# Performance work log

Hardware: AMD Instinct MI355X
Metric: run time of the kernel (lower is better)

## Reference

```python
import jax, jax.numpy as jnp
import numpy as np
from jax import lax

# hyperparams (match init_kwargs)
DIM = 192      # dim
QK = 192       # qk_dim
HEADS = 8
GS = 128       # group_size
MLP = 384      # mlp_dim
M = 64         # num_tokens
B, H, W = 4, 128, 128


def setup_inputs() -> dict:
    key = jax.random.key(0)
    ks = jax.random.split(key, 12)
    def n(k, sh, sc=0.02):
        return jax.random.normal(k, sh, dtype=jnp.float32) * sc
    return {
        "x": n(ks[0], (B, DIM, H, W), 1.0),
        "ln_g": jnp.ones((DIM,), jnp.float32),
        "ln_b": jnp.zeros((DIM,), jnp.float32),
        "Wq": n(ks[1], (DIM, QK)),
        "Wk": n(ks[2], (DIM, QK)),
        "Wv": n(ks[3], (DIM, DIM)),
        "Wproj": n(ks[4], (DIM, DIM)),
        "Wkg": n(ks[5], (DIM, QK)),      # IRCA global-key projection of means
        "Wvg": n(ks[6], (DIM, DIM)),     # IRCA global-value projection of means
        "means": n(ks[7], (M, DIM), 1.0),  # token dictionary buffer
        "Wconv": n(ks[8], (DIM, DIM)),   # 1x1 conv (no bias) as matrix
        "mlp_ln_g": jnp.ones((DIM,), jnp.float32),
        "mlp_ln_b": jnp.zeros((DIM,), jnp.float32),
        "W_fc1": n(ks[9], (DIM, MLP)),
        "dw": n(ks[10], (MLP, 1, 3, 3)),  # depthwise 3x3 in ConvFFN
        "W_fc2": n(ks[11], (MLP, DIM)),
    }


def _ln(x, g, b, eps=1e-5):
    mu = x.mean(-1, keepdims=True)
    var = ((x - mu) ** 2).mean(-1, keepdims=True)
    return (x - mu) * lax.rsqrt(var + eps) * g + b


def _attn(q, k, v):
    scale = q.shape[-1] ** -0.5
    s = jnp.einsum('...qd,...kd->...qk', q, k) * scale
    p = jax.nn.softmax(s, axis=-1)
    return jnp.einsum('...qk,...kd->...qd', p, v)


def reference(x, ln_g, ln_b, Wq, Wk, Wv, Wproj, Wkg, Wvg, means,
              Wconv, mlp_ln_g, mlp_ln_b, W_fc1, dw, W_fc2):
    b, C, h, w = x.shape
    N = h * w
    xt = x.reshape(b, C, N).transpose(0, 2, 1)          # b n c
    residual = xt
    xn = _ln(xt, ln_g, ln_b)

    # IRCA: per-head global K/V from the token dictionary (means)
    kg = (means @ Wkg).reshape(M, HEADS, QK // HEADS).transpose(1, 0, 2)   # h m dq
    vg = (means @ Wvg).reshape(M, HEADS, C // HEADS).transpose(1, 0, 2)    # h m dv

    # cluster assignment (no-grad): cosine sim to means, argsort by cluster id
    xs = lax.stop_gradient(xn)
    ms = lax.stop_gradient(means)
    xs_n = xs / (jnp.linalg.norm(xs, axis=-1, keepdims=True) + 1e-12)
    ms_n = ms / (jnp.linalg.norm(ms, axis=-1, keepdims=True) + 1e-12)
    belong = jnp.argmax(xs_n @ ms_n.T, axis=-1)          # b n
    idx = jnp.argsort(belong, axis=-1)                   # b n, cluster-sorted order

    # IASA: project, gather into cluster-sorted order
    q = jnp.take_along_axis(xn @ Wq, idx[:, :, None], axis=1)
    k = jnp.take_along_axis(xn @ Wk, idx[:, :, None], axis=1)
    v = jnp.take_along_axis(xn @ Wv, idx[:, :, None], axis=1)

    gs = min(N, GS)
    ng = (N + gs - 1) // gs
    pad_n = ng * gs - N
    pq = jnp.concatenate([q, q[:, N - pad_n:N][:, ::-1]], axis=1)
    pq = pq.reshape(b, ng, gs, HEADS, -1).transpose(0, 1, 3, 2, 4)  # b ng h gs dq

    def windows(t):
        tr = jnp.concatenate([t, t[:, N - pad_n - gs:N][:, ::-1]], axis=1)  # len ng*gs+gs
        t1 = tr[:, :ng * gs].reshape(b, ng, gs, -1)
        t2 = tr[:, gs:].reshape(b, ng, gs, -1)
        tw = jnp.concatenate([t1, t2], axis=2)           # b ng 2gs c
        return tw.reshape(b, ng, 2 * gs, HEADS, -1).transpose(0, 1, 3, 2, 4)

    kw, vw = windows(k), windows(v)
    out1 = _attn(pq, kw, vw)                             # local overlapping windows
    out2 = _attn(pq, kg[None, None], vg[None, None])     # global dictionary attention
    out = (out1 + out2).transpose(0, 1, 3, 2, 4).reshape(b, ng * gs, C)[:, :N]

    # scatter back to original token order (idx is a permutation)
    inv = jnp.argsort(idx, axis=-1)
    out = jnp.take_along_axis(out, inv[:, :, None], axis=1)
    out = (out @ Wproj) @ Wconv                           # proj + 1x1 conv (no bias)
    xt = residual + out

    # PreNorm ConvFFN: LN -> fc1 -> depthwise 3x3 -> GELU -> fc2, residual
    h1 = _ln(xt, mlp_ln_g, mlp_ln_b) @ W_fc1              # b n mlp
    himg = h1.transpose(0, 2, 1).reshape(b, MLP, h, w)
    dwc = lax.conv_general_dilated(himg, dw, (1, 1), 'SAME',
                                   feature_group_count=MLP,
                                   dimension_numbers=('NCHW', 'OIHW', 'NCHW'))
    h2 = jax.nn.gelu(dwc.reshape(b, MLP, N).transpose(0, 2, 1))
    xt = xt + h2 @ W_fc2
    return xt.transpose(0, 2, 1).reshape(b, C, h, w)
```

## Files before the change

### kernel.cpp

```cpp
#include <hip/hip_runtime.h>

using u16 = unsigned short;
using u32 = unsigned int;
typedef __attribute__((ext_vector_type(8))) short short8;
typedef __attribute__((ext_vector_type(4))) short s16x4;
typedef __attribute__((ext_vector_type(4))) float f32x4;
typedef __attribute__((ext_vector_type(2))) float f32x2;
typedef __attribute__((ext_vector_type(4))) u16 u16x4;
typedef __attribute__((ext_vector_type(4))) u32 u32x4;

constexpr int CB   = 4;
constexpr int CC   = 192;
constexpr int CN   = 16384;
constexpr int BN   = CB * CN;
constexpr int CMLP = 384;

__device__ __forceinline__ float b2f(u16 u){ return __uint_as_float(((u32)u) << 16); }
__device__ __forceinline__ u16 f2b(float f){
  u32 u = __float_as_uint(f);
  u32 r = (u + 0x7FFFu + ((u >> 16) & 1u)) >> 16;
  return (u16)r;
}
__device__ __forceinline__ short8 ld8(const u16* p) {
  s16x4 a = *(const s16x4*)p;
  s16x4 b = *(const s16x4*)(p + 4);
  short8 r;
  r[0]=a[0]; r[1]=a[1]; r[2]=a[2]; r[3]=a[3];
  r[4]=b[0]; r[5]=b[1]; r[6]=b[2]; r[7]=b[3];
  return r;
}
__device__ __forceinline__ u32 pk_bf16(float lo, float hi) {
  u32 r;
  asm("v_cvt_pk_bf16_f32 %0, %1, %2" : "=v"(r) : "v"(lo), "v"(hi));
  return r;
}
__device__ __forceinline__ float exp2_fast(float x) {
  float r;
  asm("v_exp_f32 %0, %1" : "=v"(r) : "v"(x));
  return r;
}
__device__ __forceinline__ void gl_lds16(const u16* g, u16* l) {
  __builtin_amdgcn_global_load_lds(
      (const __attribute__((address_space(1))) void*)(const void*)g,
      (__attribute__((address_space(3))) void*)(void*)l, 16, 0, 0);
}

__global__ __launch_bounds__(256) void ln_k(const float* __restrict__ src,
    const float* __restrict__ gg, const float* __restrict__ bb, u16* __restrict__ out,
    const u16* __restrict__ msnT, int* __restrict__ belong)
{
  __shared__ float t[64 * 193];
  __shared__ float sg[192], sb[192];
  __shared__ float smu[64], srs[64];
  const int tid = threadIdx.x;
  const int blk = blockIdx.x;
  const int b = blk >> 8;
  const int n0 = (blk & 255) * 64;
  if (tid < 192) { sg[tid] = gg[tid]; sb[tid] = bb[tid]; }
  const size_t sbase = ((size_t)b * CC) * CN + n0;
  #pragma unroll
  for (int it = 0; it < 48; ++it) {
    int c = it * 4 + (tid >> 6);
    int tok = tid & 63;
    t[tok * 193 + c] = src[sbase + (size_t)c * CN + tok];
  }
  __syncthreads();
  {
    int tok = tid >> 2, sub = tid & 3;
    float s = 0.f, sq = 0.f;
    #pragma unroll
    for (int i = 0; i < 48; ++i) {
      float v = t[tok * 193 + sub * 48 + i];
      s += v; sq += v * v;
    }
    s  += __shfl_xor(s, 1);  s  += __shfl_xor(s, 2);
    sq += __shfl_xor(sq, 1); sq += __shfl_xor(sq, 2);
    float mu = s * (1.f / 192.f);
    float var = fmaxf(sq * (1.f / 192.f) - mu * mu, 0.f);
    float rs = rsqrtf(var + 1e-5f);
    if (sub == 0) { smu[tok] = mu; srs[tok] = rs; }
  }
  __syncthreads();
  const size_t obase = ((size_t)(b * CN + n0)) * CC;
  #pragma unroll
  for (int it = 0; it < 48; ++it) {
    int e = it * 256 + tid;
    int tk = e / 192, c = e % 192;
    float v = (t[tk * 193 + c] - smu[tk]) * srs[tk] * sg[c] + sb[c];
    out[obase + (size_t)tk * CC + c] = f2b(v);
  }

  {
    const int wv = tid >> 6, lane = tid & 63;
    const int l15 = lane & 15, g4 = lane >> 4, q8 = g4 * 8;
    const int tok = wv * 16 + l15;
    const float mu = smu[tok], rs = srs[tok];
    short8 afm[6];
    #pragma unroll
    for (int ks = 0; ks < 6; ++ks) {
      u32x4 qq;
      #pragma unroll
      for (int j = 0; j < 4; ++j) {
        int c = ks * 32 + q8 + 2 * j;
        float v0 = (t[tok * 193 + c]     - mu) * rs * sg[c]     + sb[c];
        float v1 = (t[tok * 193 + c + 1] - mu) * rs * sg[c + 1] + sb[c + 1];
        qq[j] = pk_bf16(v0, v1);
      }
      afm[ks] = __builtin_bit_cast(short8, qq);
    }
    f32x4 sacc[4];
    #pragma unroll
    for (int ct = 0; ct < 4; ++ct) {
      sacc[ct] = 0.f;
      const u16* pM = msnT + (ct * 16 + l15) * 192 + q8;
      short8 mf[6];
      #pragma unroll
      for (int ks = 0; ks < 6; ++ks) mf[ks] = *(const short8*)(pM + ks * 32);
      #pragma unroll
      for (int ks = 0; ks < 6; ++ks)
        sacc[ct] = __builtin_amdgcn_mfma_f32_16x16x32_bf16(afm[ks], mf[ks], sacc[ct], 0, 0, 0);
    }
    #pragma unroll
    for (int r = 0; r < 4; ++r) {
      float bv = -3e38f; int bi = 1 << 30;
      #pragma unroll
      for (int ct = 0; ct < 4; ++ct) {
        float v = sacc[ct][r];
        int ci = ct * 16 + l15;
        if (v > bv || (v == bv && ci < bi)) { bv = v; bi = ci; }
      }
      #pragma unroll
      for (int d = 1; d < 16; d <<= 1) {
        float ov = __shfl_xor(bv, d);
        int   oi = __shfl_xor(bi, d);
        if (ov > bv || (ov == bv && oi < bi)) { bv = ov; bi = oi; }
      }
      if (l15 == 0) belong[b * CN + n0 + wv * 16 + g4 * 4 + r] = bi;
    }
  }
}

__global__ __launch_bounds__(256) void gemmQ_k(const u16* __restrict__ A,
    const u16* __restrict__ Wt, u16* __restrict__ qkv)
{
  __shared__ __attribute__((aligned(16))) u16 lA[64 * 192];
  const float QSC = 0.20412414523193154f * 1.4426950408889634f;
  const int tid = threadIdx.x;
  const int row0 = blockIdx.x * 64;
  const int wv = tid >> 6, lane = tid & 63;
  const int l15 = lane & 15, g4 = lane >> 4, q8 = g4 * 8;
  const int colw = wv * 144;

  #pragma unroll
  for (int j = 0; j < 6; ++j) {
    int C = (wv * 6 + j) * 64 + lane;
    int r = C / 24;
    int c = C - r * 24;
    gl_lds16(A + (size_t)(row0 + r) * 192 + c * 8, lA + (wv * 6 + j) * 512);
  }
  __syncthreads();
  short8 af[4][6];
  #pragma unroll
  for (int rt = 0; rt < 4; ++rt)
    #pragma unroll
    for (int ks = 0; ks < 6; ++ks)
      af[rt][ks] = *(const short8*)(lA + (rt * 16 + l15) * 192 + ks * 32 + q8);

  #pragma unroll
  for (int jc = 0; jc < 9; ++jc) {
    const u16* pW = Wt + (size_t)(colw + jc * 16 + l15) * 192 + q8;
    short8 wf[6];
    #pragma unroll
    for (int ks = 0; ks < 6; ++ks) wf[ks] = *(const short8*)(pW + ks * 32);
    f32x4 acc[4];
    #pragma unroll
    for (int rt = 0; rt < 4; ++rt) acc[rt] = 0.f;
    #pragma unroll
    for (int ks = 0; ks < 6; ++ks)
      #pragma unroll
      for (int rt = 0; rt < 4; ++rt)
        acc[rt] = __builtin_amdgcn_mfma_f32_16x16x32_bf16(af[rt][ks], wf[ks], acc[rt], 0, 0, 0);
    int col = colw + jc * 16 + l15;
    const float sc = (colw + jc * 16 < 192) ? QSC : 1.f;
    #pragma unroll
    for (int rt = 0; rt < 4; ++rt) {
      int row = row0 + rt * 16 + g4 * 4;
      #pragma unroll
      for (int r = 0; r < 4; ++r)
        qkv[(size_t)(row + r) * 576 + col] = f2b(acc[rt][r] * sc);
    }
  }
}

__global__ __launch_bounds__(192) void prep_means_k(const float* __restrict__ means,
    const float* __restrict__ Wkg, const float* __restrict__ Wvg,
    u16* __restrict__ msnT, float* __restrict__ kg, float* __restrict__ vg)
{
  __shared__ float sv[192];
  __shared__ float red[192];
  const int m = blockIdx.x, c = threadIdx.x;
  float v = means[m * 192 + c];
  sv[c] = v; red[c] = v * v;
  __syncthreads();
  for (int s = 96; s >= 3; s >>= 1) {
    if (c < s) red[c] += red[c + s];
    __syncthreads();
  }
  if (c == 0) red[0] = 1.f / (sqrtf(red[0] + red[1] + red[2]) + 1e-12f);
  __syncthreads();
  float scale = red[0];
  msnT[m * 192 + c] = f2b(v * scale);
  float a1 = 0.f, a2 = 0.f;
  for (int cc = 0; cc < 192; ++cc) {
    float mv = sv[cc];
    a1 += mv * Wkg[cc * 192 + c];
    a2 += mv * Wvg[cc * 192 + c];
  }
  int h = c / 24, d = c % 24;
  kg[h * (64 * 24) + m * 24 + d] = a1;
  vg[h * (64 * 24) + m * 24 + d] = a2;
}

__global__ __launch_bounds__(256) void wprep_k(
    const float* __restrict__ Wp, const float* __restrict__ Wc, u16* __restrict__ WpcT,
    const float* __restrict__ Wq, const float* __restrict__ Wk, const float* __restrict__ Wv,
    u16* __restrict__ WqkvT,
    const float* __restrict__ Wfc1, u16* __restrict__ Wfc1T,
    const float* __restrict__ Wfc2, u16* __restrict__ Wfc2T)
{
  int blk = blockIdx.x;
  int tid = threadIdx.x;
  if (blk < 144) {
    int e = blk * 256 + tid;
    if (e < 192 * 192) {
      int i = e / 192, j = e % 192;
      float a = 0.f;
      for (int k = 0; k < 192; ++k) a += Wp[i * 192 + k] * Wc[k * 192 + j];
      WpcT[j * 192 + i] = f2b(a);
    }
    return;
  }
  blk -= 144;
  if (blk < 432) {
    int which = blk / 144;
    int e = (blk % 144) * 256 + tid;
    const float* W = (which == 0) ? Wq : (which == 1) ? Wk : Wv;
    if (e < 192 * 192) {
      int j = e / 192, k = e % 192;
      WqkvT[which * 192 * 192 + e] = f2b(W[k * 192 + j]);
    }
    return;
  }
  blk -= 432;
  if (blk < 288) {
    int e = blk * 256 + tid;
    if (e < 192 * 384) {
      int j = e / 192, k = e % 192;
      Wfc1T[e] = f2b(Wfc1[k * 384 + j]);
    }
    return;
  }
  blk -= 288;
  {
    int e = blk * 256 + tid;
    if (e < 384 * 192) {
      int j = e / 384, k = e % 384;
      Wfc2T[e] = f2b(Wfc2[k * 192 + j]);
    }
  }
}

__global__ __launch_bounds__(256) void resid_k(const u16* __restrict__ qkv,
    const u16* __restrict__ WpcT, const float* __restrict__ x, u16* __restrict__ xt2,
    const float* __restrict__ g2, const float* __restrict__ b2,
    const u16* __restrict__ Wfc1T, u16* __restrict__ h1)
{
  __shared__ __attribute__((aligned(16))) u16 shraw[64 * 200];
  __shared__ float smu2[64], srs2[64];
  u16* lA    = shraw;
  u16* lnb16 = shraw;
  const int tid = threadIdx.x;
  const int row0 = blockIdx.x * 64;
  const int b = row0 >> 14;
  const int wv = tid >> 6, lane = tid & 63;
  const int l15 = lane & 15, g4 = lane >> 4, q8 = g4 * 8;

  #pragma unroll
  for (int j = 0; j < 6; ++j) {
    int C = (wv * 6 + j) * 64 + lane;
    int r = C / 24;
    int c = C - r * 24;
    const u16* gp = qkv + (size_t)(row0 + r) * 576 + c * 8;
    gl_lds16(gp, lA + (wv * 6 + j) * 512);
  }
  __syncthreads();
  short8 af[4][6];
  #pragma unroll
  for (int rt = 0; rt < 4; ++rt)
    #pragma unroll
    for (int ks = 0; ks < 6; ++ks)
      af[rt][ks] = *(const short8*)(lA + (rt * 16 + l15) * 192 + ks * 32 + q8);
  __syncthreads();

  const int colw = wv * 48;
  #pragma unroll
  for (int jc = 0; jc < 3; ++jc) {
    const u16* pW = WpcT + (size_t)(colw + jc * 16 + l15) * 192 + q8;
    short8 wf[6];
    #pragma unroll
    for (int ks = 0; ks < 6; ++ks) wf[ks] = *(const short8*)(pW + ks * 32);
    f32x4 acc[4];
    #pragma unroll
    for (int rt = 0; rt < 4; ++rt) acc[rt] = 0.f;
    #pragma unroll
    for (int ks = 0; ks < 6; ++ks)
      #pragma unroll
      for (int rt = 0; rt < 4; ++rt)
        acc[rt] = __builtin_amdgcn_mfma_f32_16x16x32_bf16(wf[ks], af[rt][ks], acc[rt], 0, 0, 0);
    #pragma unroll
    for (int rt = 0; rt < 4; ++rt) {
      int n = ((row0 + rt * 16) & 16383) + l15;
      #pragma unroll
      for (int r = 0; r < 4; ++r) {
        int col = colw + jc * 16 + g4 * 4 + r;
        size_t o2 = ((size_t)(b * CC + col)) * CN + n;
        float val = x[o2] + acc[rt][r];
        u16 vb = f2b(val);
        xt2[o2] = vb;
        lnb16[(rt * 16 + l15) * 200 + col] = vb;
      }
    }
  }
  __syncthreads();

  {
    int tok = tid >> 2, sub = tid & 3;
    float s = 0.f, sq = 0.f;
    #pragma unroll
    for (int i = 0; i < 48; ++i) {
      float v = b2f(lnb16[tok * 200 + sub * 48 + i]);
      s += v; sq += v * v;
    }
    s  += __shfl_xor(s, 1);  s  += __shfl_xor(s, 2);
    sq += __shfl_xor(sq, 1); sq += __shfl_xor(sq, 2);
    float mu = s * (1.f / 192.f);
    float var = fmaxf(sq * (1.f / 192.f) - mu * mu, 0.f);
    float rs = rsqrtf(var + 1e-5f);
    if (sub == 0) { smu2[tok] = mu; srs2[tok] = rs; }
  }
  __syncthreads();
  #pragma unroll
  for (int it = 0; it < 48; ++it) {
    int e = it * 256 + tid;
    int tk = e / 192, c = e % 192;
    float v = (b2f(lnb16[tk * 200 + c]) - smu2[tk]) * srs2[tk] * g2[c] + b2[c];
    lnb16[tk * 200 + c] = f2b(v);
  }
  __syncthreads();

  short8 af2[4][6];
  #pragma unroll
  for (int rt = 0; rt < 4; ++rt)
    #pragma unroll
    for (int ks = 0; ks < 6; ++ks)
      af2[rt][ks] = *(const short8*)(lnb16 + (rt * 16 + l15) * 200 + ks * 32 + q8);
  const int colw2 = wv * 96;
  #pragma unroll
  for (int jc = 0; jc < 6; ++jc) {
    const u16* pW = Wfc1T + (size_t)(colw2 + jc * 16 + l15) * 192 + q8;
    short8 wf[6];
    #pragma unroll
    for (int ks = 0; ks < 6; ++ks) wf[ks] = *(const short8*)(pW + ks * 32);
    f32x4 acc[4];
    #pragma unroll
    for (int rt = 0; rt < 4; ++rt) acc[rt] = 0.f;
    #pragma unroll
    for (int ks = 0; ks < 6; ++ks)
      #pragma unroll
      for (int rt = 0; rt < 4; ++rt)
        acc[rt] = __builtin_amdgcn_mfma_f32_16x16x32_bf16(af2[rt][ks], wf[ks], acc[rt], 0, 0, 0);
    int col = colw2 + jc * 16 + l15;
    #pragma unroll
    for (int rt = 0; rt < 4; ++rt) {
      int row = row0 + rt * 16 + g4 * 4;
      #pragma unroll
      for (int r = 0; r < 4; ++r)
        h1[(size_t)(row + r) * CMLP + col] = f2b(acc[rt][r]);
    }
  }
}

template<int KTOT, int NCOLS>
__global__ __launch_bounds__(256) void gemmF_k(const u16* __restrict__ A,
    const u16* __restrict__ Wt, const u16* __restrict__ resid,
    float* __restrict__ o, int astride)
{
  __shared__ __attribute__((aligned(16))) u16 lA[64 * 192];
  constexpr int KC = KTOT / 192;
  constexpr int WCOLS = NCOLS / 4;
  constexpr int WCT = WCOLS / 16;
  const int tid = threadIdx.x;
  const int row0 = blockIdx.x * 64;
  const int b = row0 >> 14;
  const int wv = tid >> 6, lane = tid & 63;
  const int l15 = lane & 15, g4 = lane >> 4, q8 = g4 * 8;
  const int colw = wv * WCOLS;

  f32x4 acc[WCT * 4];
  #pragma unroll
  for (int i = 0; i < WCT * 4; ++i) acc[i] = 0.f;

  #pragma unroll
  for (int kc = 0; kc < KC; ++kc) {
    if (kc) __syncthreads();
    #pragma unroll
    for (int j = 0; j < 6; ++j) {
      int C = (wv * 6 + j) * 64 + lane;
      int r = C / 24;
      int c = C - r * 24;
      const u16* gp = A + (size_t)(row0 + r) * astride + kc * 192 + c * 8;
      gl_lds16(gp, lA + (wv * 6 + j) * 512);
    }
    __syncthreads();
    short8 af[4][6];
    #pragma unroll
    for (int rt = 0; rt < 4; ++rt)
      #pragma unroll
      for (int ks = 0; ks < 6; ++ks)
        af[rt][ks] = *(const short8*)(lA + (rt * 16 + l15) * 192 + ks * 32 + q8);

    #pragma unroll
    for (int jc = 0; jc < WCT; ++jc) {
      const u16* pW = Wt + (size_t)(colw + jc * 16 + l15) * KTOT + kc * 192 + q8;
      short8 wf[6];
      #pragma unroll
      for (int ks = 0; ks < 6; ++ks) wf[ks] = *(const short8*)(pW + ks * 32);
      #pragma unroll
      for (int ks = 0; ks < 6; ++ks)
        #pragma unroll
        for (int rt = 0; rt < 4; ++rt)
          acc[jc * 4 + rt] = __builtin_amdgcn_mfma_f32_16x16x32_bf16(wf[ks], af[rt][ks], acc[jc * 4 + rt], 0, 0, 0);
    }
  }
  #pragma unroll
  for (int jc = 0; jc < WCT; ++jc)
    #pragma unroll
    for (int tt = 0; tt < 4; ++tt) {
      int n = ((row0 + tt * 16) & 16383) + l15;
      #pragma unroll
      for (int r = 0; r < 4; ++r) {
        int outcol = colw + jc * 16 + g4 * 4 + r;
        size_t o2 = ((size_t)(b * CC + outcol)) * CN + n;
        o[o2] = b2f(resid[o2]) + acc[jc * 4 + tt][r];
      }
    }
}

__global__ __launch_bounds__(256) void hist_k(const int* __restrict__ belong, int* __restrict__ histG)
{
  __shared__ int h[64];
  int tid = threadIdx.x, blk = blockIdx.x;
  if (tid < 64) h[tid] = 0;
  __syncthreads();
  int c = belong[blk * 256 + tid];
  atomicAdd(&h[c], 1);
  __syncthreads();
  if (tid < 64) histG[blk * 64 + tid] = h[tid];
}

__global__ __launch_bounds__(64) void scan_k(const int* __restrict__ histG, int* __restrict__ chunkBase)
{
  int b = blockIdx.x, c = threadIdx.x;
  int tot = 0;
  for (int ch = 0; ch < 64; ++ch) tot += histG[(b * 64 + ch) * 64 + c];
  int inc = tot;
  for (int d = 1; d < 64; d <<= 1) {
    int v = __shfl_up(inc, d);
    if (c >= d) inc += v;
  }
  int run = inc - tot;
  for (int ch = 0; ch < 64; ++ch) {
    chunkBase[(b * 64 + ch) * 64 + c] = run;
    run += histG[(b * 64 + ch) * 64 + c];
  }
}

__global__ __launch_bounds__(256) void rank_k(const int* __restrict__ belong,
    const int* __restrict__ chunkBase, int* __restrict__ idx)
{
  __shared__ int WH[4][64];
  int tid = threadIdx.x, blk = blockIdx.x;
  int b = blk >> 6, chl = blk & 63;
  int wv = tid >> 6, lane = tid & 63;
  ((int*)WH)[tid] = 0;
  __syncthreads();
  int nl = chl * 256 + tid;
  int c = belong[blk * 256 + tid];
  int rank = 0;
  for (int m = 0; m < 64; ++m) {
    unsigned long long msk = __ballot(c == m);
    if (c == m) {
      rank = __popcll(msk & ((1ull << lane) - 1ull));
      if (rank == 0) WH[wv][m] = __popcll(msk);
    }
  }
  __syncthreads();
  int off = 0;
  #pragma unroll
  for (int w = 0; w < 3; ++w) if (w < wv) off += WH[w][c];
  int pos = chunkBase[(b * 64 + chl) * 64 + c] + off + rank;
  idx[b * CN + pos] = nl;
}

__global__ __launch_bounds__(256) void attn_k(u16* __restrict__ qkv,
    const float* __restrict__ kg, const float* __restrict__ vg,
    const int* __restrict__ idx)
{
  __shared__ __attribute__((aligned(16))) u16 sK[320 * 24];
  __shared__ __attribute__((aligned(16))) u16 sVT[25 * 332];
  __shared__ u16 sidx[256];
  const int g = blockIdx.x, h = blockIdx.y, b = blockIdx.z;
  const int tid = threadIdx.x;
  const int wave = tid >> 6, lane = tid & 63;
  const int l15 = lane & 15, g4 = lane >> 4;
  const int q8 = g4 * 8;
  const size_t base = (size_t)b * CN * 576;
  short8 z8 = {0,0,0,0,0,0,0,0};

  {
    int p = g * 128 + tid;
    if (p >= CN) p = 2 * CN - 1 - p;
    sidx[tid] = (u16)idx[b * CN + p];
  }
  for (int e = tid; e < 332; e += 256) sVT[24 * 332 + e] = 0x3F80;
  __syncthreads();

  #pragma unroll
  for (int it = 0; it < 3; ++it) {
    int C = (it * 4 + wave) * 64 + lane;
    int r = C / 3, cs = C - r * 3;
    int p = sidx[r];
    gl_lds16(qkv + base + (size_t)p * 576 + 192 + h * 24 + cs * 8,
             sK + (it * 4 + wave) * 512);
  }
  #pragma unroll
  for (int it = 0; it < 2; ++it) {
    int e4 = (it * 256 + tid) * 4;
    if (e4 < 1536) {
      int r = e4 / 24, c = e4 % 24;
      const float* kp = kg + h * 1536 + r * 24 + c;
      u16x4 o;
      o[0] = f2b(kp[0]); o[1] = f2b(kp[1]); o[2] = f2b(kp[2]); o[3] = f2b(kp[3]);
      *(u16x4*)(sK + (256 + r) * 24 + c) = o;
    }
  }
  #pragma unroll
  for (int it = 0; it < 8; ++it) {
    int e4 = (it * 256 + tid) * 4;
    if (e4 < 7680) {
      int kk = e4 / 24, c = e4 % 24;
      if (kk < 256) {
        int p = sidx[kk];
        u16x4 v = *(const u16x4*)(qkv + base + (size_t)p * 576 + 384 + h * 24 + c);
        sVT[(c + 0) * 332 + kk] = v[0];
        sVT[(c + 1) * 332 + kk] = v[1];
        sVT[(c + 2) * 332 + kk] = v[2];
        sVT[(c + 3) * 332 + kk] = v[3];
      } else {
        const float* vp = vg + h * 1536 + (kk - 256) * 24 + c;
        sVT[(c + 0) * 332 + kk] = f2b(vp[0]);
        sVT[(c + 1) * 332 + kk] = f2b(vp[1]);
        sVT[(c + 2) * 332 + kk] = f2b(vp[2]);
        sVT[(c + 3) * 332 + kk] = f2b(vp[3]);
      }
    }
  }

  short8 qf[2];
  #pragma unroll
  for (int rt = 0; rt < 2; ++rt) {
    int qrow = sidx[wave * 32 + rt * 16 + l15];
    qf[rt] = (g4 < 3) ? ld8(qkv + base + (size_t)qrow * 576 + h * 24 + q8) : z8;
  }
  __syncthreads();

  f32x4 O1[2][2], O2[2][2];
  #pragma unroll
  for (int rt = 0; rt < 2; ++rt)
    #pragma unroll
    for (int ct2 = 0; ct2 < 2; ++ct2) { O1[rt][ct2] = 0.f; O2[rt][ct2] = 0.f; }

  const int srcLo = ((lane & 16) << 1) + l15;
  const int srcHi = srcLo + 16;
  const bool hiSel = lane >= 32;
  f32x4 zz = 0.f;

  auto do_tile = [&](int ktile, f32x4 (*O)[2]) {
    short8 aK[4];
    #pragma unroll
    for (int ct = 0; ct < 4; ++ct)
      aK[ct] = (g4 < 3) ? ld8(sK + (ktile + ct * 16 + l15) * 24 + q8) : z8;
    short8 bV[2][2];
    #pragma unroll
    for (int kc = 0; kc < 2; ++kc)
      #pragma unroll
      for (int ct2 = 0; ct2 < 2; ++ct2) {
        int vrow = ct2 * 16 + l15;
        bV[kc][ct2] = (vrow < 25) ? ld8(sVT + vrow * 332 + ktile + kc * 32 + q8) : z8;
      }
    #pragma unroll
    for (int rt = 0; rt < 2; ++rt) {
      f32x4 p[4];
      __builtin_amdgcn_s_setprio(1);
      #pragma unroll
      for (int ct = 0; ct < 4; ++ct)
        p[ct] = __builtin_amdgcn_mfma_f32_16x16x32_bf16(aK[ct], qf[rt], zz, 0, 0, 0);
      __builtin_amdgcn_s_setprio(0);
      #pragma unroll
      for (int ct = 0; ct < 4; ++ct)
        #pragma unroll
        for (int r = 0; r < 4; ++r)
          p[ct][r] = exp2_fast(p[ct][r]);
      #pragma unroll
      for (int kc = 0; kc < 2; ++kc) {
        u32 wA0 = pk_bf16(p[kc * 2][0], p[kc * 2][1]);
        u32 wA1 = pk_bf16(p[kc * 2][2], p[kc * 2][3]);
        u32 wB0 = pk_bf16(p[kc * 2 + 1][0], p[kc * 2 + 1][1]);
        u32 wB1 = pk_bf16(p[kc * 2 + 1][2], p[kc * 2 + 1][3]);
        u32 a0 = (u32)__shfl((int)wA0, srcLo), a1 = (u32)__shfl((int)wA1, srcLo);
        u32 a2 = (u32)__shfl((int)wA0, srcHi), a3 = (u32)__shfl((int)wA1, srcHi);
        u32 b0 = (u32)__shfl((int)wB0, srcLo), b1 = (u32)__shfl((int)wB1, srcLo);
        u32 b2 = (u32)__shfl((int)wB0, srcHi), b3 = (u32)__shfl((int)wB1, srcHi);
        u32x4 fr;
        fr[0] = hiSel ? b0 : a0; fr[1] = hiSel ? b1 : a1;
        fr[2] = hiSel ? b2 : a2; fr[3] = hiSel ? b3 : a3;
        short8 aP = __builtin_bit_cast(short8, fr);
        __builtin_amdgcn_s_setprio(1);
        #pragma unroll
        for (int ct2 = 0; ct2 < 2; ++ct2)
          O[rt][ct2] = __builtin_amdgcn_mfma_f32_16x16x32_bf16(aP, bV[kc][ct2], O[rt][ct2], 0, 0, 0);
        __builtin_amdgcn_s_setprio(0);
      }
    }
  };

  do_tile(0,   O1);
  do_tile(64,  O1);
  do_tile(128, O1);
  do_tile(192, O1);
  do_tile(256, O2);

  const int lsrc = (lane & 48) + 8;
  #pragma unroll
  for (int rt = 0; rt < 2; ++rt) {
    #pragma unroll
    for (int r = 0; r < 4; ++r) {
      float s1 = __shfl(O1[rt][1][r], lsrc);
      float s2 = __shfl(O2[rt][1][r], lsrc);
      float i1 = 1.f / s1;
      float i2 = 1.f / s2;
      int tok = sidx[wave * 32 + rt * 16 + g4 * 4 + r];
      #pragma unroll
      for (int ct2 = 0; ct2 < 2; ++ct2) {
        int d = ct2 * 16 + l15;
        if (d < 24) {
          float v = O1[rt][ct2][r] * i1 + O2[rt][ct2][r] * i2;
          qkv[base + (size_t)tok * 576 + h * 24 + d] = f2b(v);
        }
      }
    }
  }
}

__global__ __launch_bounds__(256) void conv_k(const u16* __restrict__ h1,
    const float* __restrict__ dw, u16* __restrict__ h2g)
{
  __shared__ float t[1156 * 10];
  __shared__ float sdw[72];
  const int tile = blockIdx.x;
  const int jg = blockIdx.y;
  const int bb = blockIdx.z;
  const int y0 = (tile >> 2) * 32, x0 = (tile & 3) * 32;
  const int tid = threadIdx.x;
  if (tid < 72) sdw[tid] = dw[jg * 72 + tid];
  #pragma unroll
  for (int it = 0; it < 5; ++it) {
    int e = it * 256 + tid;
    if (e < 1156) {
      int yy = e / 34 - 1 + y0, xx = e % 34 - 1 + x0;
      float v[8];
      if (yy >= 0 && yy < 128 && xx >= 0 && xx < 128) {
        short8 raw = *(const short8*)(h1 + ((size_t)(bb * CN + yy * 128 + xx)) * CMLP + jg * 8);
        #pragma unroll
        for (int c = 0; c < 8; ++c) v[c] = b2f((u16)raw[c]);
      } else {
        #pragma unroll
        for (int c = 0; c < 8; ++c) v[c] = 0.f;
      }
      #pragma unroll
      for (int c = 0; c < 8; c += 2) {
        f32x2 p; p[0] = v[c]; p[1] = v[c + 1];
        *(f32x2*)(t + e * 10 + c) = p;
      }
    }
  }
  __syncthreads();
  float acc[4][8];
  #pragma unroll
  for (int px = 0; px < 4; ++px)
    #pragma unroll
    for (int c = 0; c < 8; ++c) acc[px][c] = 0.f;
  #pragma unroll
  for (int k = 0; k < 9; ++k) {
    const int dy = k / 3, dx = k % 3;
    float w[8];
    #pragma unroll
    for (int c = 0; c < 8; ++c) w[c] = sdw[c * 9 + k];
    #pragma unroll
    for (int px = 0; px < 4; ++px) {
      int idx2 = px * 256 + tid;
      int oy = idx2 >> 5, ox = idx2 & 31;
      const float* vp = t + ((oy + dy) * 34 + ox + dx) * 10;
      #pragma unroll
      for (int c = 0; c < 8; ++c) acc[px][c] += vp[c] * w[c];
    }
  }
  #pragma unroll
  for (int px = 0; px < 4; ++px) {
    int idx2 = px * 256 + tid;
    int oy = idx2 >> 5, ox = idx2 & 31;
    short8 o;
    #pragma unroll
    for (int c = 0; c < 8; ++c) {
      float a = acc[px][c];
      float u = 1.5957691216057308f * (a + 0.044715f * a * a * a);
      float gel = a / (1.f + __expf(-u));
      o[c] = (short)f2b(gel);
    }
    *(short8*)(h2g + ((size_t)(bb * CN + (y0 + oy) * 128 + x0 + ox)) * CMLP + jg * 8) = o;
  }
}

extern "C" void kernel_launch(void* const* d_in, const int* in_sizes, int n_in,
                              void* d_out, int out_size, void* d_ws, size_t ws_size,
                              hipStream_t stream)
{
  const float* x     = (const float*)d_in[0];
  const float* ln_g  = (const float*)d_in[1];
  const float* ln_b  = (const float*)d_in[2];
  const float* Wq    = (const float*)d_in[3];
  const float* Wk    = (const float*)d_in[4];
  const float* Wv    = (const float*)d_in[5];
  const float* Wproj = (const float*)d_in[6];
  const float* Wkg   = (const float*)d_in[7];
  const float* Wvg   = (const float*)d_in[8];
  const float* means = (const float*)d_in[9];
  const float* Wconv = (const float*)d_in[10];
  const float* mlp_g = (const float*)d_in[11];
  const float* mlp_b = (const float*)d_in[12];
  const float* Wfc1  = (const float*)d_in[13];
  const float* dw    = (const float*)d_in[14];
  const float* Wfc2  = (const float*)d_in[15];
  float* out = (float*)d_out;
  (void)in_sizes; (void)n_in; (void)out_size; (void)ws_size;

  char* ws = (char*)d_ws;
  size_t off = 0;
  auto alloc = [&](size_t sz) { void* p = ws + off; off += (sz + 255) & ~(size_t)255; return p; };
  u16*  xn    = (u16*)alloc((size_t)BN * 192 * 2);
  u16*  qkv   = (u16*)alloc((size_t)BN * 576 * 2);
  u16*  xt2   = (u16*)alloc((size_t)BN * 192 * 2);
  u16*  h1    = (u16*)alloc((size_t)BN * 384 * 2);
  u16*  h2g   = (u16*)alloc((size_t)BN * 384 * 2);
  u16*  msnT  = (u16*)alloc(64 * 192 * 2);
  u16*  WqkvT = (u16*)alloc(576 * 192 * 2);
  u16*  WpcT  = (u16*)alloc(192 * 192 * 2);
  u16*  Wfc1T = (u16*)alloc(384 * 192 * 2);
  u16*  Wfc2T = (u16*)alloc(192 * 384 * 2);
  float* kg   = (float*)alloc(8 * 64 * 24 * 4);
  float* vg   = (float*)alloc(8 * 64 * 24 * 4);
  int*  belong = (int*)alloc(BN * 4);
  int*  idxb   = (int*)alloc(BN * 4);
  int*  histG  = (int*)alloc(256 * 64 * 4);
  int*  chunkBase = (int*)alloc(256 * 64 * 4);

  prep_means_k<<<64, 192, 0, stream>>>(means, Wkg, Wvg, msnT, kg, vg);
  wprep_k<<<1152, 256, 0, stream>>>(Wproj, Wconv, WpcT, Wq, Wk, Wv, WqkvT,
                                    Wfc1, Wfc1T, Wfc2, Wfc2T);

  ln_k<<<1024, 256, 0, stream>>>(x, ln_g, ln_b, xn, msnT, belong);
  hist_k<<<256, 256, 0, stream>>>(belong, histG);
  scan_k<<<4, 64, 0, stream>>>(histG, chunkBase);
  rank_k<<<256, 256, 0, stream>>>(belong, chunkBase, idxb);
  gemmQ_k<<<1024, 256, 0, stream>>>(xn, WqkvT, qkv);
  attn_k<<<dim3(128, 8, 4), 256, 0, stream>>>(qkv, kg, vg, idxb);
  resid_k<<<1024, 256, 0, stream>>>(qkv, WpcT, x, xt2, mlp_g, mlp_b, Wfc1T, h1);
  conv_k<<<dim3(16, 48, 4), 256, 0, stream>>>(h1, dw, h2g);
  gemmF_k<384, 192><<<1024, 256, 0, stream>>>(h2g, Wfc2T, xt2, out, 384);
}
```

Before: 303.5 us.

## Scatter K/V into cluster-sorted order in QKV GEMM for contiguous attention loads

rank_k now also writes the inverse permutation, and the QKV GEMM scatters K and V rows directly into cluster-sorted positions in a separate kv buffer. Q stays in token order in its own buffer. The attention kernel can then read its overlapping K/V windows as contiguous rows instead of gathering them through idx. The cost of random access moves from the attention loads to scattered GEMM stores, and the change adds one extra int buffer.

```diff
diff --git a/kernel.cpp b/kernel.cpp
--- a/kernel.cpp
+++ b/kernel.cpp
@@ -141,16 +141,20 @@
 }
 
 __global__ __launch_bounds__(256) void gemmQ_k(const u16* __restrict__ A,
-    const u16* __restrict__ Wt, u16* __restrict__ qkv)
+    const u16* __restrict__ Wt, const int* __restrict__ inv,
+    u16* __restrict__ qo, u16* __restrict__ kv)
 {
   __shared__ __attribute__((aligned(16))) u16 lA[64 * 192];
+  __shared__ int sInv[64];
   const float QSC = 0.20412414523193154f * 1.4426950408889634f;
   const int tid = threadIdx.x;
   const int row0 = blockIdx.x * 64;
+  const int b = row0 >> 14;
   const int wv = tid >> 6, lane = tid & 63;
   const int l15 = lane & 15, g4 = lane >> 4, q8 = g4 * 8;
   const int colw = wv * 144;
 
+  if (tid < 64) sInv[tid] = inv[row0 + tid];
   #pragma unroll
   for (int j = 0; j < 6; ++j) {
     int C = (wv * 6 + j) * 64 + lane;
@@ -166,6 +170,7 @@
     for (int ks = 0; ks < 6; ++ks)
       af[rt][ks] = *(const short8*)(lA + (rt * 16 + l15) * 192 + ks * 32 + q8);
 
+  const size_t kvb = (size_t)b * CN * 384;
   #pragma unroll
   for (int jc = 0; jc < 9; ++jc) {
     const u16* pW = Wt + (size_t)(colw + jc * 16 + l15) * 192 + q8;
@@ -181,13 +186,24 @@
       for (int rt = 0; rt < 4; ++rt)
         acc[rt] = __builtin_amdgcn_mfma_f32_16x16x32_bf16(af[rt][ks], wf[ks], acc[rt], 0, 0, 0);
     int col = colw + jc * 16 + l15;
-    const float sc = (colw + jc * 16 < 192) ? QSC : 1.f;
-    #pragma unroll
-    for (int rt = 0; rt < 4; ++rt) {
-      int row = row0 + rt * 16 + g4 * 4;
-      #pragma unroll
-      for (int r = 0; r < 4; ++r)
-        qkv[(size_t)(row + r) * 576 + col] = f2b(acc[rt][r] * sc);
+    if (colw + jc * 16 < 192) {
+      #pragma unroll
+      for (int rt = 0; rt < 4; ++rt) {
+        int row = row0 + rt * 16 + g4 * 4;
+        #pragma unroll
+        for (int r = 0; r < 4; ++r)
+          qo[(size_t)(row + r) * 192 + col] = f2b(acc[rt][r] * QSC);
+      }
+    } else {
+      #pragma unroll
+      for (int rt = 0; rt < 4; ++rt) {
+        int rloc = rt * 16 + g4 * 4;
+        #pragma unroll
+        for (int r = 0; r < 4; ++r) {
+          int pos = sInv[rloc + r];
+          kv[kvb + (size_t)pos * 384 + (col - 192)] = f2b(acc[rt][r]);
+        }
+      }
     }
   }
 }
@@ -270,7 +286,7 @@
   }
 }
 
-__global__ __launch_bounds__(256) void resid_k(const u16* __restrict__ qkv,
+__global__ __launch_bounds__(256) void resid_k(const u16* __restrict__ qo,
     const u16* __restrict__ WpcT, const float* __restrict__ x, u16* __restrict__ xt2,
     const float* __restrict__ g2, const float* __restrict__ b2,
     const u16* __restrict__ Wfc1T, u16* __restrict__ h1)
@@ -290,7 +306,7 @@
     int C = (wv * 6 + j) * 64 + lane;
     int r = C / 24;
     int c = C - r * 24;
-    const u16* gp = qkv + (size_t)(row0 + r) * 576 + c * 8;
+    const u16* gp = qo + (size_t)(row0 + r) * 192 + c * 8;
     gl_lds16(gp, lA + (wv * 6 + j) * 512);
   }
   __syncthreads();
@@ -486,7 +502,7 @@
 }
 
 __global__ __launch_bounds__(256) void rank_k(const int* __restrict__ belong,
-    const int* __restrict__ chunkBase, int* __restrict__ idx)
+    const int* __restrict__ chunkBase, int* __restrict__ idx, int* __restrict__ inv)
 {
   __shared__ int WH[4][64];
   int tid = threadIdx.x, blk = blockIdx.x;
@@ -510,9 +526,11 @@
   for (int w = 0; w < 3; ++w) if (w < wv) off += WH[w][c];
   int pos = chunkBase[(b * 64 + chl) * 64 + c] + off + rank;
   idx[b * CN + pos] = nl;
-}
-
-__global__ __launch_bounds__(256) void attn_k(u16* __restrict__ qkv,
+  inv[b * CN + nl] = pos;
+}
+
+__global__ __launch_bounds__(256) void attn_k(u16* __restrict__ qo,
+    const u16* __restrict__ kv,
     const float* __restrict__ kg, const float* __restrict__ vg,
     const int* __restrict__ idx)
 {
@@ -524,7 +542,8 @@
   const int wave = tid >> 6, lane = tid & 63;
   const int l15 = lane & 15, g4 = lane >> 4;
   const int q8 = g4 * 8;
-  const size_t base = (size_t)b * CN * 576;
+  const size_t qob = (size_t)b * CN * 192;
+  const size_t kvb = (size_t)b * CN * 384;
   short8 z8 = {0,0,0,0,0,0,0,0};
 
   {
@@ -539,8 +558,9 @@
   for (int it = 0; it < 3; ++it) {
     int C = (it * 4 + wave) * 64 + lane;
     int r = C / 3, cs = C - r * 3;
-    int p = sidx[r];
-    gl_lds16(qkv + base + (size_t)p * 576 + 192 + h * 24 + cs * 8,
+    int p = g * 128 + r;
+    if (p >= CN) p = 2 * CN - 1 - p;
+    gl_lds16(kv + kvb + (size_t)p * 384 + h * 24 + cs * 8,
              sK + (it * 4 + wave) * 512);
   }
   #pragma unroll
@@ -560,8 +580,9 @@
     if (e4 < 7680) {
       int kk = e4 / 24, c = e4 % 24;
       if (kk < 256) {
-        int p = sidx[kk];
-        u16x4 v = *(const u16x4*)(qkv + base + (size_t)p * 576 + 384 + h * 24 + c);
+        int p = g * 128 + kk;
+        if (p >= CN) p = 2 * CN - 1 - p;
+        u16x4 v = *(const u16x4*)(kv + kvb + (size_t)p * 384 + 192 + h * 24 + c);
         sVT[(c + 0) * 332 + kk] = v[0];
         sVT[(c + 1) * 332 + kk] = v[1];
         sVT[(c + 2) * 332 + kk] = v[2];
@@ -580,7 +601,7 @@
   #pragma unroll
   for (int rt = 0; rt < 2; ++rt) {
     int qrow = sidx[wave * 32 + rt * 16 + l15];
-    qf[rt] = (g4 < 3) ? ld8(qkv + base + (size_t)qrow * 576 + h * 24 + q8) : z8;
+    qf[rt] = (g4 < 3) ? ld8(qo + qob + (size_t)qrow * 192 + h * 24 + q8) : z8;
   }
   __syncthreads();
 
@@ -665,7 +686,7 @@
         int d = ct2 * 16 + l15;
         if (d < 24) {
           float v = O1[rt][ct2][r] * i1 + O2[rt][ct2][r] * i2;
-          qkv[base + (size_t)tok * 576 + h * 24 + d] = f2b(v);
+          qo[qob + (size_t)tok * 192 + h * 24 + d] = f2b(v);
         }
       }
     }
@@ -768,7 +789,8 @@
   size_t off = 0;
   auto alloc = [&](size_t sz) { void* p = ws + off; off += (sz + 255) & ~(size_t)255; return p; };
   u16*  xn    = (u16*)alloc((size_t)BN * 192 * 2);
-  u16*  qkv   = (u16*)alloc((size_t)BN * 576 * 2);
+  u16*  qo    = (u16*)alloc((size_t)BN * 192 * 2);
+  u16*  kvb   = (u16*)alloc((size_t)BN * 384 * 2);
   u16*  xt2   = (u16*)alloc((size_t)BN * 192 * 2);
   u16*  h1    = (u16*)alloc((size_t)BN * 384 * 2);
   u16*  h2g   = (u16*)alloc((size_t)BN * 384 * 2);
@@ -781,6 +803,7 @@
   float* vg   = (float*)alloc(8 * 64 * 24 * 4);
   int*  belong = (int*)alloc(BN * 4);
   int*  idxb   = (int*)alloc(BN * 4);
+  int*  invb   = (int*)alloc(BN * 4);
   int*  histG  = (int*)alloc(256 * 64 * 4);
   int*  chunkBase = (int*)alloc(256 * 64 * 4);
 
@@ -791,10 +814,10 @@
   ln_k<<<1024, 256, 0, stream>>>(x, ln_g, ln_b, xn, msnT, belong);
   hist_k<<<256, 256, 0, stream>>>(belong, histG);
   scan_k<<<4, 64, 0, stream>>>(histG, chunkBase);
-  rank_k<<<256, 256, 0, stream>>>(belong, chunkBase, idxb);
-  gemmQ_k<<<1024, 256, 0, stream>>>(xn, WqkvT, qkv);
-  attn_k<<<dim3(128, 8, 4), 256, 0, stream>>>(qkv, kg, vg, idxb);
-  resid_k<<<1024, 256, 0, stream>>>(qkv, WpcT, x, xt2, mlp_g, mlp_b, Wfc1T, h1);
+  rank_k<<<256, 256, 0, stream>>>(belong, chunkBase, idxb, invb);
+  gemmQ_k<<<1024, 256, 0, stream>>>(xn, WqkvT, invb, qo, kvb);
+  attn_k<<<dim3(128, 8, 4), 256, 0, stream>>>(qo, kvb, kg, vg, idxb);
+  resid_k<<<1024, 256, 0, stream>>>(qo, WpcT, x, xt2, mlp_g, mlp_b, Wfc1T, h1);
   conv_k<<<dim3(16, 48, 4), 256, 0, stream>>>(h1, dw, h2g);
   gemmF_k<384, 192><<<1024, 256, 0, stream>>>(h2g, Wfc2T, xt2, out, 384);
 }
```

New measurement: 315.1 us. 3.8% more time.
